# Kernel optimization log

Hardware: AMD Instinct MI355X
Metric: run time of the kernel (lower is better)

The kernel has to match this reference:

```python
import jax, jax.numpy as jnp
import numpy as np

N_NODES = 100000
N_EDGES = 1600000
D_IN, D_H, D_OUT = 256, 128, 128


def setup_inputs() -> dict:
    key = jax.random.key(0)
    ks = jax.random.split(key, 8)
    x = jax.random.normal(ks[0], (N_NODES, D_IN), dtype=jnp.float32)
    edge_index = jax.random.randint(ks[1], (2, N_EDGES), 0, N_NODES, dtype=jnp.int64)
    def glorot(k, fan_in, fan_out):
        s = jnp.sqrt(6.0 / (fan_in + fan_out))
        return jax.random.uniform(k, (fan_in, fan_out), jnp.float32, -s, s)
    W1 = glorot(ks[2], D_IN, D_H)
    b1 = jnp.zeros((D_H,), jnp.float32)
    W2 = glorot(ks[3], D_H, D_H)
    b2 = jnp.zeros((D_H,), jnp.float32)
    W3 = glorot(ks[4], D_H, D_OUT)
    b3 = jnp.zeros((D_OUT,), jnp.float32)
    return {"x": x, "edge_index": edge_index,
            "W1": W1, "b1": b1, "W2": W2, "b2": b2, "W3": W3, "b3": b3}


def _gcn_norm(edge_index, n_nodes):
    # PyG GCNConv: add self-loops, symmetric normalization D^-1/2 (A+I) D^-1/2
    loop = jnp.arange(n_nodes, dtype=edge_index.dtype)
    src = jnp.concatenate([edge_index[0], loop])  # source j
    dst = jnp.concatenate([edge_index[1], loop])  # target i
    deg = jax.ops.segment_sum(jnp.ones_like(dst, dtype=jnp.float32), dst,
                              num_segments=n_nodes)
    dinv = jnp.where(deg > 0, jax.lax.rsqrt(deg), 0.0)
    norm = dinv[src] * dinv[dst]  # [E+N]
    return src, dst, norm


def _gcn_conv(h, W, b, src, dst, norm, n_nodes):
    h = h @ W                                   # [N, d_out] transform first
    msg = h[src] * norm[:, None]                # gather + edge-weight
    out = jax.ops.segment_sum(msg, dst, num_segments=n_nodes)  # scatter-add
    return out + b


def reference(x, edge_index, W1, b1, W2, b2, W3, b3):
    n = x.shape[0]
    src, dst, norm = _gcn_norm(edge_index, n)
    h = jax.nn.relu(_gcn_conv(x, W1, b1, src, dst, norm, n))
    h = jax.nn.relu(_gcn_conv(h, W2, b2, src, dst, norm, n))
    return _gcn_conv(h, W3, b3, src, dst, norm, n)
```

## Files before the change

### kernel.cpp

```cpp
#include <hip/hip_runtime.h>
#include <hip/hip_fp16.h>
#include <math.h>


#define N_NODES 100000
#define N_EDGES 1600000

typedef _Float16 f16x8 __attribute__((ext_vector_type(8)));
typedef float    f32x4 __attribute__((ext_vector_type(4)));


__global__ __launch_bounds__(256) void k_zero_int(int* __restrict__ p, int n) {
    int i = blockIdx.x * 256 + threadIdx.x;
    if (i < n) p[i] = 0;
}

__global__ __launch_bounds__(256) void k_scan_block(const int* __restrict__ cnt, int* __restrict__ excl,
                                                    int* __restrict__ bsum, int n) {
    __shared__ int s[256];
    int i = blockIdx.x * 256 + threadIdx.x;
    int v = (i < n) ? ((cnt[i] + 7) & ~7) : 0;
    s[threadIdx.x] = v;
    __syncthreads();
    #pragma unroll
    for (int off = 1; off < 256; off <<= 1) {
        int t = (threadIdx.x >= (unsigned)off) ? s[threadIdx.x - off] : 0;
        __syncthreads();
        s[threadIdx.x] += t;
        __syncthreads();
    }
    if (i < n) excl[i] = s[threadIdx.x] - v;
    if (threadIdx.x == 255) bsum[blockIdx.x] = s[255];
}

__global__ __launch_bounds__(512) void k_scan_partials(int* __restrict__ bsum, int nb) {
    __shared__ int s[512];
    int tid = threadIdx.x;
    int v = (tid < nb) ? bsum[tid] : 0;
    s[tid] = v;
    __syncthreads();
    #pragma unroll
    for (int off = 1; off < 512; off <<= 1) {
        int t = (tid >= (unsigned)off) ? s[tid - off] : 0;
        __syncthreads();
        s[tid] += t;
        __syncthreads();
    }
    if (tid < nb) bsum[tid] = s[tid] - v;
}

__global__ __launch_bounds__(256) void k_finalize(const int* __restrict__ excl, const int* __restrict__ bsum,
                                                  const int* __restrict__ cnt, int* __restrict__ rowptr,
                                                  int* __restrict__ fill, float* __restrict__ dinv, int n) {
    int i = blockIdx.x * 256 + threadIdx.x;
    if (i < n) {
        int rp = excl[i] + bsum[i >> 8];
        rowptr[i] = rp;
        fill[i]   = rp;
        dinv[i]   = rsqrtf((float)(cnt[i] + 1));
    }
}

__global__ __launch_bounds__(256) void k_init_csr(int* __restrict__ csr, int n, unsigned int* __restrict__ phz,
                                                  float* __restrict__ dinvN) {
    int i = blockIdx.x * 256 + threadIdx.x;
    if (i < n) csr[i] = N_NODES;
    if (blockIdx.x == 0 && threadIdx.x < 64) phz[threadIdx.x] = 0;
    if (blockIdx.x == 0 && threadIdx.x == 64) dinvN[0] = 0.f;
}

__global__ __launch_bounds__(256) void k_fill_edges(const int* __restrict__ src, const int* __restrict__ dst,
                                                    int* __restrict__ fill, int* __restrict__ csr,
                                                    int E, int lo, int hi) {
    int e = blockIdx.x * 256 + threadIdx.x;
    if (e < E) {
        int d = dst[e];
        if (d >= lo && d < hi) {
            int p = atomicAdd(&fill[d], 1);
            csr[p] = src[e];
        }
    }
}

__global__ __launch_bounds__(256) void k_wpack(const float* __restrict__ W, _Float16* __restrict__ Wpk, int K) {
    int j = blockIdx.x * 256 + threadIdx.x;
    if (j < K * 128) {
        int i  = j & 7;
        int l  = (j >> 3) & 63;
        int tc = (j >> 9) & 7;
        int c  = j >> 12;
        int col = tc * 16 + (l & 15);
        int k   = c * 32 + (l >> 4) * 8 + i;
        float w = W[(size_t)k * 128 + col];
        _Float16 h = (_Float16)w;
        Wpk[j] = h;
        Wpk[(size_t)K * 128 + j] = (_Float16)(w - (float)h);
    }
}


template <int K>
__global__ __launch_bounds__(256) void k_gemm1_count(const float* __restrict__ X,
                                                     const _Float16* __restrict__ Wpk,
                                                     _Float16* __restrict__ Y, int n,
                                                     const int* __restrict__ dst, int* __restrict__ cnt,
                                                     int E, int gemm_blocks) {
    constexpr int NS = K / 64;
    __shared__ float sX[64 * 64];
    if ((int)blockIdx.x >= gemm_blocks) {
        int e = (blockIdx.x - gemm_blocks) * 256 + threadIdx.x;
        if (e < E) atomicAdd(&cnt[dst[e]], 1);
        return;
    }
    const int t    = threadIdx.x;
    const int wave = t >> 6;
    const int lane = t & 63;
    const int lrow = lane & 15;
    const int kgrp = lane >> 4;
    const int row0 = blockIdx.x * 64;
    const int R    = wave * 16 + lrow;
    const _Float16* __restrict__ Wlo = Wpk + (size_t)K * 128;

    const int gsl = t & 15;
    const int rb  = t >> 4;
    const int r0 = rb, r1 = rb + 16, r2 = rb + 32, r3 = rb + 48;
    const int gc0 = ((gsl & 8) + ((gsl & 7) ^ (r0 & 7))) << 2;
    const int gc1 = ((gsl & 8) + ((gsl & 7) ^ (r1 & 7))) << 2;
    const int gc2 = ((gsl & 8) + ((gsl & 7) ^ (r2 & 7))) << 2;
    const int gc3 = ((gsl & 8) + ((gsl & 7) ^ (r3 & 7))) << 2;
    const bool ok0 = row0 + r0 < n, ok1 = row0 + r1 < n;
    const bool ok2 = row0 + r2 < n, ok3 = row0 + r3 < n;
    const float* __restrict__ xr0 = X + (size_t)(row0 + r0) * K;
    const float* __restrict__ xr1 = X + (size_t)(row0 + r1) * K;
    const float* __restrict__ xr2 = X + (size_t)(row0 + r2) * K;
    const float* __restrict__ xr3 = X + (size_t)(row0 + r3) * K;

    f32x4 acc[8];
    #pragma unroll
    for (int i = 0; i < 8; ++i) acc[i] = (f32x4){0.f, 0.f, 0.f, 0.f};

    const float4 z4 = make_float4(0.f, 0.f, 0.f, 0.f);
    float4 rv0 = ok0 ? *(const float4*)&xr0[gc0] : z4;
    float4 rv1 = ok1 ? *(const float4*)&xr1[gc1] : z4;
    float4 rv2 = ok2 ? *(const float4*)&xr2[gc2] : z4;
    float4 rv3 = ok3 ? *(const float4*)&xr3[gc3] : z4;
    *(float4*)&sX[(r0 * 16 + gsl) * 4] = rv0;
    *(float4*)&sX[(r1 * 16 + gsl) * 4] = rv1;
    *(float4*)&sX[(r2 * 16 + gsl) * 4] = rv2;
    *(float4*)&sX[(r3 * 16 + gsl) * 4] = rv3;
    __syncthreads();

    #pragma unroll
    for (int s = 0; s < NS; ++s) {
        if (s + 1 < NS) {
            const int o = (s + 1) * 64;
            rv0 = ok0 ? *(const float4*)&xr0[o + gc0] : z4;
            rv1 = ok1 ? *(const float4*)&xr1[o + gc1] : z4;
            rv2 = ok2 ? *(const float4*)&xr2[o + gc2] : z4;
            rv3 = ok3 ? *(const float4*)&xr3[o + gc3] : z4;
        }
        #pragma unroll
        for (int cc = 0; cc < 2; ++cc) {
            const int c = s * 2 + cc;
            float4 x0 = *(const float4*)&sX[(R * 16 + cc * 8 + ((kgrp * 2)     ^ (R & 7))) * 4];
            float4 x1 = *(const float4*)&sX[(R * 16 + cc * 8 + ((kgrp * 2 + 1) ^ (R & 7))) * 4];
            float xs[8] = {x0.x, x0.y, x0.z, x0.w, x1.x, x1.y, x1.z, x1.w};
            f16x8 ah, al;
            #pragma unroll
            for (int i = 0; i < 8; ++i) {
                _Float16 h = (_Float16)xs[i];
                ah[i] = h;
                al[i] = (_Float16)(xs[i] - (float)h);
            }
            const size_t wb = ((size_t)(c * 8) * 64 + lane) * 8;
            #pragma unroll
            for (int tc = 0; tc < 8; ++tc) {
                f16x8 bh = *(const f16x8*)(Wpk + wb + (size_t)tc * 512);
                f16x8 bl = *(const f16x8*)(Wlo + wb + (size_t)tc * 512);
                acc[tc] = __builtin_amdgcn_mfma_f32_16x16x32_f16(ah, bh, acc[tc], 0, 0, 0);
                acc[tc] = __builtin_amdgcn_mfma_f32_16x16x32_f16(al, bh, acc[tc], 0, 0, 0);
                acc[tc] = __builtin_amdgcn_mfma_f32_16x16x32_f16(ah, bl, acc[tc], 0, 0, 0);
            }
        }
        if (s + 1 < NS) {
            __syncthreads();
            *(float4*)&sX[(r0 * 16 + gsl) * 4] = rv0;
            *(float4*)&sX[(r1 * 16 + gsl) * 4] = rv1;
            *(float4*)&sX[(r2 * 16 + gsl) * 4] = rv2;
            *(float4*)&sX[(r3 * 16 + gsl) * 4] = rv3;
            __syncthreads();
        }
    }

    #pragma unroll
    for (int r = 0; r < 4; ++r) {
        int grow = row0 + wave * 16 + kgrp * 4 + r;
        if (grow < n) {
            _Float16* yr = Y + (size_t)grow * 128 + lrow;
            #pragma unroll
            for (int tc = 0; tc < 8; ++tc) yr[tc * 16] = (_Float16)acc[tc][r];
        }
    }
}


template <int K>
__global__ __launch_bounds__(256) void k_gemm_f16(const _Float16* __restrict__ X,
                                                  const _Float16* __restrict__ Wpk,
                                                  _Float16* __restrict__ Y, int n) {
    constexpr int NC = K / 32;
    __shared__ unsigned int sX[64 * 20];
    const int t    = threadIdx.x;
    const int wave = t >> 6;
    const int lane = t & 63;
    const int lrow = lane & 15;
    const int kgrp = lane >> 4;
    const int row0 = blockIdx.x * 64;
    const int R    = wave * 16 + lrow;
    const _Float16* __restrict__ Wlo = Wpk + (size_t)K * 128;

    const int sr = t >> 2, sg = t & 3;
    const bool sok = row0 + sr < n;
    const unsigned int* __restrict__ xrow = (const unsigned int*)(X + (size_t)(row0 + sr) * K);

    f32x4 acc[8];
    #pragma unroll
    for (int i = 0; i < 8; ++i) acc[i] = (f32x4){0.f, 0.f, 0.f, 0.f};

    const uint4 zu = make_uint4(0, 0, 0, 0);
    uint4 rv = sok ? *(const uint4*)&xrow[sg * 4] : zu;
    *(uint4*)&sX[sr * 20 + sg * 4] = rv;
    __syncthreads();

    #pragma unroll
    for (int c = 0; c < NC; ++c) {
        if (c + 1 < NC) rv = sok ? *(const uint4*)&xrow[(c + 1) * 16 + sg * 4] : zu;
        f16x8 a = *(const f16x8*)&sX[R * 20 + kgrp * 4];
        const size_t wb = ((size_t)(c * 8) * 64 + lane) * 8;
        #pragma unroll
        for (int tc = 0; tc < 8; ++tc) {
            f16x8 bh = *(const f16x8*)(Wpk + wb + (size_t)tc * 512);
            f16x8 bl = *(const f16x8*)(Wlo + wb + (size_t)tc * 512);
            acc[tc] = __builtin_amdgcn_mfma_f32_16x16x32_f16(a, bh, acc[tc], 0, 0, 0);
            acc[tc] = __builtin_amdgcn_mfma_f32_16x16x32_f16(a, bl, acc[tc], 0, 0, 0);
        }
        if (c + 1 < NC) {
            __syncthreads();
            *(uint4*)&sX[sr * 20 + sg * 4] = rv;
            __syncthreads();
        }
    }

    #pragma unroll
    for (int r = 0; r < 4; ++r) {
        int grow = row0 + wave * 16 + kgrp * 4 + r;
        if (grow < n) {
            _Float16* yr = Y + (size_t)grow * 128 + lrow;
            #pragma unroll
            for (int tc = 0; tc < 8; ++tc) yr[tc * 16] = (_Float16)acc[tc][r];
        }
    }
}


__device__ __forceinline__ void facc8(float a[8], uint4 u, float w) {
    float2 p;
    p = __half22float2(*(__half2*)&u.x); a[0] = fmaf(w, p.x, a[0]); a[1] = fmaf(w, p.y, a[1]);
    p = __half22float2(*(__half2*)&u.y); a[2] = fmaf(w, p.x, a[2]); a[3] = fmaf(w, p.y, a[3]);
    p = __half22float2(*(__half2*)&u.z); a[4] = fmaf(w, p.x, a[4]); a[5] = fmaf(w, p.y, a[5]);
    p = __half22float2(*(__half2*)&u.w); a[6] = fmaf(w, p.x, a[6]); a[7] = fmaf(w, p.y, a[7]);
}

template <bool RELU, bool OUTF16>
__global__ __launch_bounds__(256) void k_agg(const __half* __restrict__ H, const int* __restrict__ rowptr,
                                             const int* __restrict__ cnt, const int* __restrict__ csr,
                                             const float* __restrict__ dinv, const float* __restrict__ bias,
                                             void* __restrict__ out, int n) {
    const int lane  = threadIdx.x & 63;
    const int q     = lane >> 4;
    const int fl    = lane & 15;
    const int wave0 = (int)((blockIdx.x * 256 + threadIdx.x) >> 6);
    const int nwave = (int)((gridDim.x * 256) >> 6);
    const uint4* __restrict__ Hu = (const uint4*)H;
    const float4 b0 = *(const float4*)&bias[fl * 8];
    const float4 b1 = *(const float4*)&bias[fl * 8 + 4];

    const int nquad = n >> 2;
    for (int g = wave0; g < nquad; g += nwave) {
        const int node = g * 4 + q;
        const float dv = dinv[node];
        float a[8];
        {
            uint4 u = Hu[(size_t)node * 16 + fl];
            float2 p;
            p = __half22float2(*(__half2*)&u.x); a[0] = dv * p.x; a[1] = dv * p.y;
            p = __half22float2(*(__half2*)&u.y); a[2] = dv * p.x; a[3] = dv * p.y;
            p = __half22float2(*(__half2*)&u.z); a[4] = dv * p.x; a[5] = dv * p.y;
            p = __half22float2(*(__half2*)&u.w); a[6] = dv * p.x; a[7] = dv * p.y;
        }

        const int c0 = rowptr[node];
        const int cn = cnt[node];
        for (int e8 = 0; e8 < cn; e8 += 8) {
            const int4* qp = (const int4*)(csr + c0 + e8);
            int4 qa = qp[0], qb = qp[1];
            uint4 u0 = Hu[(size_t)qa.x * 16 + fl];
            uint4 u1 = Hu[(size_t)qa.y * 16 + fl];
            uint4 u2 = Hu[(size_t)qa.z * 16 + fl];
            uint4 u3 = Hu[(size_t)qa.w * 16 + fl];
            uint4 u4 = Hu[(size_t)qb.x * 16 + fl];
            uint4 u5 = Hu[(size_t)qb.y * 16 + fl];
            uint4 u6 = Hu[(size_t)qb.z * 16 + fl];
            uint4 u7 = Hu[(size_t)qb.w * 16 + fl];
            float d0 = dinv[qa.x], d1 = dinv[qa.y], d2 = dinv[qa.z], d3 = dinv[qa.w];
            float d4 = dinv[qb.x], d5 = dinv[qb.y], d6 = dinv[qb.z], d7 = dinv[qb.w];
            facc8(a, u0, d0); facc8(a, u1, d1); facc8(a, u2, d2); facc8(a, u3, d3);
            facc8(a, u4, d4); facc8(a, u5, d5); facc8(a, u6, d6); facc8(a, u7, d7);
        }

        float o[8];
        o[0] = fmaf(dv, a[0], b0.x); o[1] = fmaf(dv, a[1], b0.y);
        o[2] = fmaf(dv, a[2], b0.z); o[3] = fmaf(dv, a[3], b0.w);
        o[4] = fmaf(dv, a[4], b1.x); o[5] = fmaf(dv, a[5], b1.y);
        o[6] = fmaf(dv, a[6], b1.z); o[7] = fmaf(dv, a[7], b1.w);
        if (RELU) {
            #pragma unroll
            for (int i = 0; i < 8; ++i) o[i] = fmaxf(o[i], 0.f);
        }
        if (OUTF16) {
            f16x8 hv;
            #pragma unroll
            for (int i = 0; i < 8; ++i) hv[i] = (_Float16)o[i];
            *(f16x8*)((_Float16*)out + (size_t)node * 128 + fl * 8) = hv;
        } else {
            float* op = (float*)out + (size_t)node * 128 + fl * 8;
            *(float4*)&op[0] = make_float4(o[0], o[1], o[2], o[3]);
            *(float4*)&op[4] = make_float4(o[4], o[5], o[6], o[7]);
        }
    }
}


extern "C" void kernel_launch(void* const* d_in, const int* in_sizes, int n_in,
                              void* d_out, int out_size, void* d_ws, size_t ws_size,
                              hipStream_t stream) {
    const float* x  = (const float*)d_in[0];
    const int*   ei = (const int*)d_in[1];
    const float* W1 = (const float*)d_in[2];
    const float* b1 = (const float*)d_in[3];
    const float* W2 = (const float*)d_in[4];
    const float* b2 = (const float*)d_in[5];
    const float* W3 = (const float*)d_in[6];
    const float* b3 = (const float*)d_in[7];
    float* out = (float*)d_out;

    const int N = N_NODES, E = N_EDGES;
    const int EP = E + 7 * N + 64;
    const int* src = ei;
    const int* dst = ei + E;

    char* w = (char*)d_ws;
    auto alloc = [&](size_t bytes) -> void* {
        void* p = (void*)w;
        w += (bytes + 255) & ~(size_t)255;
        return p;
    };
    int*      cnt    = (int*)alloc((size_t)N * 4);
    int*      excl   = (int*)alloc((size_t)N * 4);
    int*      bsum   = (int*)alloc(4096);
    int*      rowptr = (int*)alloc((size_t)N * 4);
    int*      fill   = (int*)alloc((size_t)N * 4);
    float*    dinv   = (float*)alloc((size_t)(N + 8) * 4);
    int*      csr    = (int*)alloc((size_t)EP * 4);
    _Float16* Ph     = (_Float16*)alloc((size_t)(N + 8) * 128 * 2);
    _Float16* Qh     = (_Float16*)alloc((size_t)N * 128 * 2);
    _Float16* Wpk    = (_Float16*)alloc((size_t)2 * 256 * 128 * 2);

    const int nbN = (N + 255) / 256;
    const int nbE = (E + 255) / 256;
    const int nbP = (EP + 255) / 256;
    const int gemm_grid = (N + 63) / 64;
    const int agg_grid  = 2048;

    k_zero_int<<<nbN, 256, 0, stream>>>(cnt, N);
    k_wpack<<<(256 * 128 + 255) / 256, 256, 0, stream>>>(W1, Wpk, 256);
    k_gemm1_count<256><<<gemm_grid + nbE, 256, 0, stream>>>(x, Wpk, Ph, N, dst, cnt, E, gemm_grid);

    k_scan_block<<<nbN, 256, 0, stream>>>(cnt, excl, bsum, N);
    k_scan_partials<<<1, 512, 0, stream>>>(bsum, nbN);
    k_finalize<<<nbN, 256, 0, stream>>>(excl, bsum, cnt, rowptr, fill, dinv, N);
    k_init_csr<<<nbP, 256, 0, stream>>>(csr, EP, (unsigned int*)(Ph + (size_t)N * 128), dinv + N);
    for (int r = 0; r < 4; ++r) {
        int lo = r * (N / 4);
        int hi = (r == 3) ? N : (r + 1) * (N / 4);
        k_fill_edges<<<nbE, 256, 0, stream>>>(src, dst, fill, csr, E, lo, hi);
    }

    k_agg<true, true><<<agg_grid, 256, 0, stream>>>((const __half*)Ph, rowptr, cnt, csr, dinv, b1, Qh, N);
    k_wpack<<<(128 * 128 + 255) / 256, 256, 0, stream>>>(W2, Wpk, 128);
    k_gemm_f16<128><<<gemm_grid, 256, 0, stream>>>(Qh, Wpk, Ph, N);
    k_agg<true, true><<<agg_grid, 256, 0, stream>>>((const __half*)Ph, rowptr, cnt, csr, dinv, b2, Qh, N);
    k_wpack<<<(128 * 128 + 255) / 256, 256, 0, stream>>>(W3, Wpk, 128);
    k_gemm_f16<128><<<gemm_grid, 256, 0, stream>>>(Qh, Wpk, Ph, N);
    k_agg<false, false><<<agg_grid, 256, 0, stream>>>((const __half*)Ph, rowptr, cnt, csr, dinv, b3, out, N);
}
```

Measured before the change: 442.4 us.

## Fuse aggregation with following GEMM, staging aggregated rows in shared memory

Layers 1 and 2 now aggregate and transform in one kernel. Each block aggregates 64 nodes into an LDS tile of half-precision rows and then runs the MFMA GEMM straight from LDS. This drops the intermediate Qh write and read-back and two kernel launches per layer. A second ping-pong feature buffer and separate packed weight buffers let all weight packing be hoisted before the layer chain. The cost is that the fused kernel uses a one-block-per-64-rows grid instead of the persistent grid-stride aggregation. Its gather latency can no longer be balanced across waves the same way, and the larger LDS footprint may reduce occupancy.

```diff
diff --git a/kernel.cpp b/kernel.cpp
--- a/kernel.cpp
+++ b/kernel.cpp
@@ -61,12 +61,15 @@
     }
 }
 
-__global__ __launch_bounds__(256) void k_init_csr(int* __restrict__ csr, int n, unsigned int* __restrict__ phz,
+__global__ __launch_bounds__(256) void k_init_csr(int* __restrict__ csr, int n,
+                                                  unsigned int* __restrict__ phz,
+                                                  unsigned int* __restrict__ phz2,
                                                   float* __restrict__ dinvN) {
     int i = blockIdx.x * 256 + threadIdx.x;
     if (i < n) csr[i] = N_NODES;
-    if (blockIdx.x == 0 && threadIdx.x < 64) phz[threadIdx.x] = 0;
-    if (blockIdx.x == 0 && threadIdx.x == 64) dinvN[0] = 0.f;
+    if (blockIdx.x == 0 && threadIdx.x < 64)  phz [threadIdx.x] = 0;
+    if (blockIdx.x == 0 && threadIdx.x >= 64 && threadIdx.x < 128) phz2[threadIdx.x - 64] = 0;
+    if (blockIdx.x == 0 && threadIdx.x == 128) dinvN[0] = 0.f;
 }
 
 __global__ __launch_bounds__(256) void k_fill_edges(const int* __restrict__ src, const int* __restrict__ dst,
@@ -204,38 +207,98 @@
 }
 
 
-template <int K>
-__global__ __launch_bounds__(256) void k_gemm_f16(const _Float16* __restrict__ X,
+__device__ __forceinline__ void facc8(float a[8], uint4 u, float w) {
+    float2 p;
+    p = __half22float2(*(__half2*)&u.x); a[0] = fmaf(w, p.x, a[0]); a[1] = fmaf(w, p.y, a[1]);
+    p = __half22float2(*(__half2*)&u.y); a[2] = fmaf(w, p.x, a[2]); a[3] = fmaf(w, p.y, a[3]);
+    p = __half22float2(*(__half2*)&u.z); a[4] = fmaf(w, p.x, a[4]); a[5] = fmaf(w, p.y, a[5]);
+    p = __half22float2(*(__half2*)&u.w); a[6] = fmaf(w, p.x, a[6]); a[7] = fmaf(w, p.y, a[7]);
+}
+
+__device__ __forceinline__ void agg_node(const uint4* __restrict__ Hu, const int* __restrict__ rowptr,
+                                         const int* __restrict__ cnt, const int* __restrict__ csr,
+                                         const float* __restrict__ dinv, const float4 b0, const float4 b1,
+                                         int node, int fl, bool relu, float o[8]) {
+    const float dv = dinv[node];
+    float a[8];
+    {
+        uint4 u = Hu[(size_t)node * 16 + fl];
+        float2 p;
+        p = __half22float2(*(__half2*)&u.x); a[0] = dv * p.x; a[1] = dv * p.y;
+        p = __half22float2(*(__half2*)&u.y); a[2] = dv * p.x; a[3] = dv * p.y;
+        p = __half22float2(*(__half2*)&u.z); a[4] = dv * p.x; a[5] = dv * p.y;
+        p = __half22float2(*(__half2*)&u.w); a[6] = dv * p.x; a[7] = dv * p.y;
+    }
+    const int c0 = rowptr[node];
+    const int cn = cnt[node];
+    for (int e8 = 0; e8 < cn; e8 += 8) {
+        const int4* qp = (const int4*)(csr + c0 + e8);
+        int4 qa = qp[0], qb = qp[1];
+        uint4 u0 = Hu[(size_t)qa.x * 16 + fl];
+        uint4 u1 = Hu[(size_t)qa.y * 16 + fl];
+        uint4 u2 = Hu[(size_t)qa.z * 16 + fl];
+        uint4 u3 = Hu[(size_t)qa.w * 16 + fl];
+        uint4 u4 = Hu[(size_t)qb.x * 16 + fl];
+        uint4 u5 = Hu[(size_t)qb.y * 16 + fl];
+        uint4 u6 = Hu[(size_t)qb.z * 16 + fl];
+        uint4 u7 = Hu[(size_t)qb.w * 16 + fl];
+        float d0 = dinv[qa.x], d1 = dinv[qa.y], d2 = dinv[qa.z], d3 = dinv[qa.w];
+        float d4 = dinv[qb.x], d5 = dinv[qb.y], d6 = dinv[qb.z], d7 = dinv[qb.w];
+        facc8(a, u0, d0); facc8(a, u1, d1); facc8(a, u2, d2); facc8(a, u3, d3);
+        facc8(a, u4, d4); facc8(a, u5, d5); facc8(a, u6, d6); facc8(a, u7, d7);
+    }
+    o[0] = fmaf(dv, a[0], b0.x); o[1] = fmaf(dv, a[1], b0.y);
+    o[2] = fmaf(dv, a[2], b0.z); o[3] = fmaf(dv, a[3], b0.w);
+    o[4] = fmaf(dv, a[4], b1.x); o[5] = fmaf(dv, a[5], b1.y);
+    o[6] = fmaf(dv, a[6], b1.z); o[7] = fmaf(dv, a[7], b1.w);
+    if (relu) {
+        #pragma unroll
+        for (int i = 0; i < 8; ++i) o[i] = fmaxf(o[i], 0.f);
+    }
+}
+
+
+__global__ __launch_bounds__(256) void k_agg_gemm(const __half* __restrict__ H,
+                                                  const int* __restrict__ rowptr, const int* __restrict__ cnt,
+                                                  const int* __restrict__ csr, const float* __restrict__ dinv,
+                                                  const float* __restrict__ bias,
                                                   const _Float16* __restrict__ Wpk,
                                                   _Float16* __restrict__ Y, int n) {
-    constexpr int NC = K / 32;
-    __shared__ unsigned int sX[64 * 20];
+    constexpr int K = 128;
+    __shared__ unsigned int sQ[64 * 68];
     const int t    = threadIdx.x;
     const int wave = t >> 6;
     const int lane = t & 63;
+    const int q    = lane >> 4;
+    const int fl   = lane & 15;
+    const int row0 = blockIdx.x * 64;
+    const uint4* __restrict__ Hu = (const uint4*)H;
+    const float4 b0 = *(const float4*)&bias[fl * 8];
+    const float4 b1 = *(const float4*)&bias[fl * 8 + 4];
+
+    #pragma unroll
+    for (int p = 0; p < 4; ++p) {
+        const int lr   = wave * 16 + p * 4 + q;
+        const int node = row0 + lr;
+        float o[8] = {0.f, 0.f, 0.f, 0.f, 0.f, 0.f, 0.f, 0.f};
+        if (node < n)
+            agg_node(Hu, rowptr, cnt, csr, dinv, b0, b1, node, fl, true, o);
+        f16x8 hv;
+        #pragma unroll
+        for (int i = 0; i < 8; ++i) hv[i] = (_Float16)o[i];
+        *(uint4*)&sQ[lr * 68 + fl * 4] = *(uint4*)&hv;
+    }
+
     const int lrow = lane & 15;
     const int kgrp = lane >> 4;
-    const int row0 = blockIdx.x * 64;
-    const int R    = wave * 16 + lrow;
     const _Float16* __restrict__ Wlo = Wpk + (size_t)K * 128;
-
-    const int sr = t >> 2, sg = t & 3;
-    const bool sok = row0 + sr < n;
-    const unsigned int* __restrict__ xrow = (const unsigned int*)(X + (size_t)(row0 + sr) * K);
-
     f32x4 acc[8];
     #pragma unroll
     for (int i = 0; i < 8; ++i) acc[i] = (f32x4){0.f, 0.f, 0.f, 0.f};
 
-    const uint4 zu = make_uint4(0, 0, 0, 0);
-    uint4 rv = sok ? *(const uint4*)&xrow[sg * 4] : zu;
-    *(uint4*)&sX[sr * 20 + sg * 4] = rv;
-    __syncthreads();
-
-    #pragma unroll
-    for (int c = 0; c < NC; ++c) {
-        if (c + 1 < NC) rv = sok ? *(const uint4*)&xrow[(c + 1) * 16 + sg * 4] : zu;
-        f16x8 a = *(const f16x8*)&sX[R * 20 + kgrp * 4];
+    #pragma unroll
+    for (int c = 0; c < K / 32; ++c) {
+        f16x8 a = *(const f16x8*)&sQ[(wave * 16 + lrow) * 68 + c * 16 + kgrp * 4];
         const size_t wb = ((size_t)(c * 8) * 64 + lane) * 8;
         #pragma unroll
         for (int tc = 0; tc < 8; ++tc) {
@@ -244,11 +307,6 @@
             acc[tc] = __builtin_amdgcn_mfma_f32_16x16x32_f16(a, bh, acc[tc], 0, 0, 0);
             acc[tc] = __builtin_amdgcn_mfma_f32_16x16x32_f16(a, bl, acc[tc], 0, 0, 0);
         }
-        if (c + 1 < NC) {
-            __syncthreads();
-            *(uint4*)&sX[sr * 20 + sg * 4] = rv;
-            __syncthreads();
-        }
     }
 
     #pragma unroll
@@ -263,19 +321,10 @@
 }
 
 
-__device__ __forceinline__ void facc8(float a[8], uint4 u, float w) {
-    float2 p;
-    p = __half22float2(*(__half2*)&u.x); a[0] = fmaf(w, p.x, a[0]); a[1] = fmaf(w, p.y, a[1]);
-    p = __half22float2(*(__half2*)&u.y); a[2] = fmaf(w, p.x, a[2]); a[3] = fmaf(w, p.y, a[3]);
-    p = __half22float2(*(__half2*)&u.z); a[4] = fmaf(w, p.x, a[4]); a[5] = fmaf(w, p.y, a[5]);
-    p = __half22float2(*(__half2*)&u.w); a[6] = fmaf(w, p.x, a[6]); a[7] = fmaf(w, p.y, a[7]);
-}
-
-template <bool RELU, bool OUTF16>
-__global__ __launch_bounds__(256) void k_agg(const __half* __restrict__ H, const int* __restrict__ rowptr,
-                                             const int* __restrict__ cnt, const int* __restrict__ csr,
-                                             const float* __restrict__ dinv, const float* __restrict__ bias,
-                                             void* __restrict__ out, int n) {
+__global__ __launch_bounds__(256) void k_agg_final(const __half* __restrict__ H, const int* __restrict__ rowptr,
+                                                   const int* __restrict__ cnt, const int* __restrict__ csr,
+                                                   const float* __restrict__ dinv, const float* __restrict__ bias,
+                                                   float* __restrict__ out, int n) {
     const int lane  = threadIdx.x & 63;
     const int q     = lane >> 4;
     const int fl    = lane & 15;
@@ -288,55 +337,11 @@
     const int nquad = n >> 2;
     for (int g = wave0; g < nquad; g += nwave) {
         const int node = g * 4 + q;
-        const float dv = dinv[node];
-        float a[8];
-        {
-            uint4 u = Hu[(size_t)node * 16 + fl];
-            float2 p;
-            p = __half22float2(*(__half2*)&u.x); a[0] = dv * p.x; a[1] = dv * p.y;
-            p = __half22float2(*(__half2*)&u.y); a[2] = dv * p.x; a[3] = dv * p.y;
-            p = __half22float2(*(__half2*)&u.z); a[4] = dv * p.x; a[5] = dv * p.y;
-            p = __half22float2(*(__half2*)&u.w); a[6] = dv * p.x; a[7] = dv * p.y;
-        }
-
-        const int c0 = rowptr[node];
-        const int cn = cnt[node];
-        for (int e8 = 0; e8 < cn; e8 += 8) {
-            const int4* qp = (const int4*)(csr + c0 + e8);
-            int4 qa = qp[0], qb = qp[1];
-            uint4 u0 = Hu[(size_t)qa.x * 16 + fl];
-            uint4 u1 = Hu[(size_t)qa.y * 16 + fl];
-            uint4 u2 = Hu[(size_t)qa.z * 16 + fl];
-            uint4 u3 = Hu[(size_t)qa.w * 16 + fl];
-            uint4 u4 = Hu[(size_t)qb.x * 16 + fl];
-            uint4 u5 = Hu[(size_t)qb.y * 16 + fl];
-            uint4 u6 = Hu[(size_t)qb.z * 16 + fl];
-            uint4 u7 = Hu[(size_t)qb.w * 16 + fl];
-            float d0 = dinv[qa.x], d1 = dinv[qa.y], d2 = dinv[qa.z], d3 = dinv[qa.w];
-            float d4 = dinv[qb.x], d5 = dinv[qb.y], d6 = dinv[qb.z], d7 = dinv[qb.w];
-            facc8(a, u0, d0); facc8(a, u1, d1); facc8(a, u2, d2); facc8(a, u3, d3);
-            facc8(a, u4, d4); facc8(a, u5, d5); facc8(a, u6, d6); facc8(a, u7, d7);
-        }
-
         float o[8];
-        o[0] = fmaf(dv, a[0], b0.x); o[1] = fmaf(dv, a[1], b0.y);
-        o[2] = fmaf(dv, a[2], b0.z); o[3] = fmaf(dv, a[3], b0.w);
-        o[4] = fmaf(dv, a[4], b1.x); o[5] = fmaf(dv, a[5], b1.y);
-        o[6] = fmaf(dv, a[6], b1.z); o[7] = fmaf(dv, a[7], b1.w);
-        if (RELU) {
-            #pragma unroll
-            for (int i = 0; i < 8; ++i) o[i] = fmaxf(o[i], 0.f);
-        }
-        if (OUTF16) {
-            f16x8 hv;
-            #pragma unroll
-            for (int i = 0; i < 8; ++i) hv[i] = (_Float16)o[i];
-            *(f16x8*)((_Float16*)out + (size_t)node * 128 + fl * 8) = hv;
-        } else {
-            float* op = (float*)out + (size_t)node * 128 + fl * 8;
-            *(float4*)&op[0] = make_float4(o[0], o[1], o[2], o[3]);
-            *(float4*)&op[4] = make_float4(o[4], o[5], o[6], o[7]);
-        }
+        agg_node(Hu, rowptr, cnt, csr, dinv, b0, b1, node, fl, false, o);
+        float* op = out + (size_t)node * 128 + fl * 8;
+        *(float4*)&op[0] = make_float4(o[0], o[1], o[2], o[3]);
+        *(float4*)&op[4] = make_float4(o[4], o[5], o[6], o[7]);
     }
 }
 
@@ -373,8 +378,10 @@
     float*    dinv   = (float*)alloc((size_t)(N + 8) * 4);
     int*      csr    = (int*)alloc((size_t)EP * 4);
     _Float16* Ph     = (_Float16*)alloc((size_t)(N + 8) * 128 * 2);
-    _Float16* Qh     = (_Float16*)alloc((size_t)N * 128 * 2);
-    _Float16* Wpk    = (_Float16*)alloc((size_t)2 * 256 * 128 * 2);
+    _Float16* Ph2    = (_Float16*)alloc((size_t)(N + 8) * 128 * 2);
+    _Float16* Wpk1   = (_Float16*)alloc((size_t)2 * 256 * 128 * 2);
+    _Float16* Wpk2   = (_Float16*)alloc((size_t)2 * 128 * 128 * 2);
+    _Float16* Wpk3   = (_Float16*)alloc((size_t)2 * 128 * 128 * 2);
 
     const int nbN = (N + 255) / 256;
     const int nbE = (E + 255) / 256;
@@ -383,24 +390,24 @@
     const int agg_grid  = 2048;
 
     k_zero_int<<<nbN, 256, 0, stream>>>(cnt, N);
-    k_wpack<<<(256 * 128 + 255) / 256, 256, 0, stream>>>(W1, Wpk, 256);
-    k_gemm1_count<256><<<gemm_grid + nbE, 256, 0, stream>>>(x, Wpk, Ph, N, dst, cnt, E, gemm_grid);
+    k_wpack<<<(256 * 128 + 255) / 256, 256, 0, stream>>>(W1, Wpk1, 256);
+    k_gemm1_count<256><<<gemm_grid + nbE, 256, 0, stream>>>(x, Wpk1, Ph, N, dst, cnt, E, gemm_grid);
 
     k_scan_block<<<nbN, 256, 0, stream>>>(cnt, excl, bsum, N);
     k_scan_partials<<<1, 512, 0, stream>>>(bsum, nbN);
     k_finalize<<<nbN, 256, 0, stream>>>(excl, bsum, cnt, rowptr, fill, dinv, N);
-    k_init_csr<<<nbP, 256, 0, stream>>>(csr, EP, (unsigned int*)(Ph + (size_t)N * 128), dinv + N);
+    k_init_csr<<<nbP, 256, 0, stream>>>(csr, EP, (unsigned int*)(Ph + (size_t)N * 128),
+                                        (unsigned int*)(Ph2 + (size_t)N * 128), dinv + N);
     for (int r = 0; r < 4; ++r) {
         int lo = r * (N / 4);
         int hi = (r == 3) ? N : (r + 1) * (N / 4);
         k_fill_edges<<<nbE, 256, 0, stream>>>(src, dst, fill, csr, E, lo, hi);
     }
 
-    k_agg<true, true><<<agg_grid, 256, 0, stream>>>((const __half*)Ph, rowptr, cnt, csr, dinv, b1, Qh, N);
-    k_wpack<<<(128 * 128 + 255) / 256, 256, 0, stream>>>(W2, Wpk, 128);
-    k_gemm_f16<128><<<gemm_grid, 256, 0, stream>>>(Qh, Wpk, Ph, N);
-    k_agg<true, true><<<agg_grid, 256, 0, stream>>>((const __half*)Ph, rowptr, cnt, csr, dinv, b2, Qh, N);
-    k_wpack<<<(128 * 128 + 255) / 256, 256, 0, stream>>>(W3, Wpk, 128);
-    k_gemm_f16<128><<<gemm_grid, 256, 0, stream>>>(Qh, Wpk, Ph, N);
-    k_agg<false, false><<<agg_grid, 256, 0, stream>>>((const __half*)Ph, rowptr, cnt, csr, dinv, b3, out, N);
-}
+    k_wpack<<<(128 * 128 + 255) / 256, 256, 0, stream>>>(W2, Wpk2, 128);
+    k_wpack<<<(128 * 128 + 255) / 256, 256, 0, stream>>>(W3, Wpk3, 128);
+
+    k_agg_gemm<<<gemm_grid, 256, 0, stream>>>((const __half*)Ph,  rowptr, cnt, csr, dinv, b1, Wpk2, Ph2, N);
+    k_agg_gemm<<<gemm_grid, 256, 0, stream>>>((const __half*)Ph2, rowptr, cnt, csr, dinv, b2, Wpk3, Ph,  N);
+    k_agg_final<<<agg_grid, 256, 0, stream>>>((const __half*)Ph, rowptr, cnt, csr, dinv, b3, out, N);
+}
```

After: 439.9 us. About the same (-0.5%).
